# Optimization experiments

Hardware: AMD Instinct MI355X
Metric: run time of the kernel (lower is better)

Reference implementation:

```python
import jax, jax.numpy as jnp
import numpy as np

D_EMBEDDING = 512
DIMENSION = 64
B, N = 8, 2048


def setup_inputs() -> dict:
    key = jax.random.key(0)
    k1, k2, k3, k4, k5, k6 = jax.random.split(key, 6)
    bound = 1.0 / np.sqrt(D_EMBEDDING)  # nn.Linear default init
    return {
        "key_input": jax.random.normal(k1, (B, N, D_EMBEDDING), jnp.float32),
        "query_input": jax.random.normal(k2, (B, N, D_EMBEDDING), jnp.float32),
        "value_input": jax.random.normal(k3, (B, N, D_EMBEDDING), jnp.float32),
        "padding_mask": jnp.zeros((B, 1, N), dtype=bool),
        "masked_attention": 1,
        "W_key": jax.random.uniform(k4, (D_EMBEDDING, DIMENSION), jnp.float32, -bound, bound),
        "W_query": jax.random.uniform(k5, (D_EMBEDDING, DIMENSION), jnp.float32, -bound, bound),
        "W_value": jax.random.uniform(k6, (D_EMBEDDING, DIMENSION), jnp.float32, -bound, bound),
    }


def reference(key_input, query_input, value_input, padding_mask, masked_attention,
              W_key, W_query, W_value):
    # NOTE: faithful to the original torch code, which uses self.key for
    # Q, K AND V (W_query / W_value are unused by forward) and scales by
    # sqrt(D_i) where D_i is the INPUT embedding dim (512), not the head dim.
    B_, N_, D_i = value_input.shape
    K = key_input @ W_key      # [B, N, d]
    Q = query_input @ W_key    # [B, N, d]
    V = value_input @ W_key    # [B, N, d]

    scores = jnp.einsum("bqd,bkd->bqk", Q, K) / jnp.sqrt(jnp.float32(D_i))
    neg_inf = jnp.float32(-jnp.inf)
    scores = jnp.where(padding_mask, neg_inf, scores)
    if masked_attention:
        causal = jnp.tril(jnp.ones((N_, N_), dtype=bool))  # [N, N]
        scores = jnp.where(causal, scores, neg_inf)
    probs = jax.nn.softmax(scores, axis=-1)
    return jnp.einsum("bqk,bkd->bqd", probs, V)
```

## Files before the change

### kernel.cpp

```cpp
#include <hip/hip_runtime.h>
#include <hip/hip_bf16.h>
#include <math.h>

#define D_EMB 512
#define HD 64
#define BB 8
#define NN 2048
#define MROWS (BB*NN)

typedef short short8  __attribute__((ext_vector_type(8)));
typedef short short4v __attribute__((ext_vector_type(4)));
typedef float f32x4   __attribute__((ext_vector_type(4)));

#define QSCALE 0.063758708f

__device__ __forceinline__ short f2bf(float x){
    unsigned u = __float_as_uint(x);
    unsigned r = (u + 0x7fffu + ((u >> 16) & 1u)) >> 16;
    return (short)r;
}
__device__ __forceinline__ float bf2f(short b){
    return __uint_as_float(((unsigned)(unsigned short)b) << 16);
}
__device__ __forceinline__ unsigned pkbf(float a, float b){
    __hip_bfloat162 h = __float22bfloat162_rn(make_float2(a, b));
    unsigned u; __builtin_memcpy(&u, &h, 4); return u;
}
__device__ __forceinline__ void gl16(const short* g, short* l){
    __builtin_amdgcn_global_load_lds(
        (const __attribute__((address_space(1))) unsigned*)g,
        (__attribute__((address_space(3))) unsigned*)l, 16, 0, 0);
}

__global__ __launch_bounds__(256)
void wt_kernel(const float* __restrict__ W, short* __restrict__ Wtf){
    for (int idx = blockIdx.x * 256 + threadIdx.x; idx < D_EMB*HD; idx += 64*256){
        int k = idx >> 6, n = idx & 63;
        int off = (((k >> 5)*4 + (n >> 4))*64 + ((k >> 3) & 3)*16 + (n & 15))*8 + (k & 7);
        Wtf[off] = f2bf(W[idx]);
    }
}

__global__ __launch_bounds__(256, 2)
void proj_kernel(const float* __restrict__ Xq, const float* __restrict__ Xk,
                 const float* __restrict__ Xv, const short* __restrict__ Wtf,
                 short* __restrict__ Qb, short* __restrict__ Kb,
                 short* __restrict__ Vt)
{
    __shared__ short sW[D_EMB*HD];
    const int tid = threadIdx.x;
    const int lane = tid & 63;
    const int lc = lane & 15, quad = lane >> 4;
    const int wid = blockIdx.x * 4 + (tid >> 6);
    const int m0 = wid * 16;
    const int tensor = m0 >> 14;
    const int rloc = m0 & (MROWS - 1);
    const float* X = (tensor == 0) ? Xq : (tensor == 1 ? Xk : Xv);
    const float* xbase = X + (size_t)(rloc + lc)*D_EMB + quad*8;

    float4 xa[4][2];
#pragma unroll
    for (int p = 0; p < 4; ++p){
        xa[p][0] = *(const float4*)(xbase + p*32);
        xa[p][1] = *(const float4*)(xbase + p*32 + 4);
    }

#pragma unroll
    for (int pass = 0; pass < 16; ++pass)
        gl16(Wtf + pass*2048 + tid*8, sW + pass*2048 + tid*8);

    f32x4 acc[4];
#pragma unroll
    for (int t = 0; t < 4; ++t)
#pragma unroll
        for (int r = 0; r < 4; ++r) acc[t][r] = 0.f;

    __syncthreads();

#pragma unroll
    for (int c16 = 0; c16 < 16; ++c16){
        float4 f0 = xa[c16 & 3][0], f1 = xa[c16 & 3][1];
        if (c16 < 12){
            xa[c16 & 3][0] = *(const float4*)(xbase + (c16+4)*32);
            xa[c16 & 3][1] = *(const float4*)(xbase + (c16+4)*32 + 4);
        }
        union { short8 s8; unsigned u[4]; } a;
        a.u[0] = pkbf(f0.x, f0.y); a.u[1] = pkbf(f0.z, f0.w);
        a.u[2] = pkbf(f1.x, f1.y); a.u[3] = pkbf(f1.z, f1.w);
#pragma unroll
        for (int t = 0; t < 4; ++t){
            short8 bf = *(const short8*)&sW[((c16*4 + t)*64 + lane)*8];
            acc[t] = __builtin_amdgcn_mfma_f32_16x16x32_bf16(a.s8, bf, acc[t], 0,0,0);
        }
    }

    if (tensor == 0){
#pragma unroll
        for (int t = 0; t < 4; ++t)
#pragma unroll
            for (int r = 0; r < 4; ++r)
                Qb[(size_t)(rloc + quad*4 + r)*HD + t*16 + lc] = f2bf(acc[t][r] * QSCALE);
    } else if (tensor == 1){
#pragma unroll
        for (int t = 0; t < 4; ++t)
#pragma unroll
            for (int r = 0; r < 4; ++r){
                const int R = rloc + quad*4 + r;
                const int nin = R & 63;
                const int off = ((R >> 6) << 12) + nin*64
                              + ((((t << 1) | (lc >> 3)) ^ (nin & 7)) << 3) + (lc & 7);
                Kb[off] = f2bf(acc[t][r]);
            }
    } else {
#pragma unroll
        for (int t = 0; t < 4; ++t)
#pragma unroll
            for (int r = 0; r < 4; ++r){
                const int R = rloc + quad*4 + r;
                const int nin = R & 63;
                const int d = t*16 + lc;
                const int off = ((R >> 6) << 12) + d*64
                              + (((nin >> 3) ^ (lc & 7)) << 3) + (nin & 7);
                Vt[off] = f2bf(acc[t][r]);
            }
    }
}

template<int SH>
__global__ __launch_bounds__(256)
void attn_part(const short* __restrict__ Qb, const short* __restrict__ Kb,
               const short* __restrict__ Vt, const unsigned char* __restrict__ pad,
               const int* __restrict__ mflag, float* __restrict__ out,
               float* __restrict__ Lp, short* __restrict__ Op)
{
    constexpr int M   = 1 << SH;
    constexpr int NG  = 32 / M;
    constexpr int UPB = M * NG * (NG + 1) / 2;
    constexpr int PPB = UPB - M;

    __shared__ short sK[2][4096];
    __shared__ short sV[2][4096];
    __shared__ short sP[4][16][80];

    const int tid = threadIdx.x, lane = tid & 63, lc = lane & 15, quad = lane >> 4, w = tid >> 6;
    const int unit = blockIdx.x;
    const int b = unit / UPB;
    const int rem = unit - b * UPB;
    int a = 0;
    while (rem >= (M * (a + 1) * (a + 2)) / 2) ++a;
    const int u = rem - M * a * (a + 1) / 2;
    const int C = a + 1;
    const int r = u / C, c = u - r * C;
    const int j = a * M + r;
    const int q0 = j * 64;

    const bool causal = (mflag[0] != 0);
    const int T = causal ? (j + 1) : 32;
    const int qq = (T + C - 1) / C;
    const int t0 = c * qq;
    const int t1 = min(t0 + qq, T);
    const int tb = b * 32;
    const unsigned char* padb = pad + (size_t)b * NN;

    const short* qrow = Qb + ((size_t)b * NN + q0 + w*16 + lc) * HD;
    const short8 qf0 = *(const short8*)(qrow + quad * 8);
    const short8 qf1 = *(const short8*)(qrow + 32 + quad * 8);

    f32x4 o[4];
#pragma unroll
    for (int t = 0; t < 4; ++t)
#pragma unroll
        for (int rr = 0; rr < 4; ++rr) o[t][rr] = 0.f;
    float lacc = 0.f;

    {
        const short* gk = Kb + ((size_t)(tb + t0) << 12) + w*1024 + lane*8;
        const short* gv = Vt + ((size_t)(tb + t0) << 12) + w*1024 + lane*8;
        short* lk = &sK[0][w*1024 + lane*8];
        short* lv = &sV[0][w*1024 + lane*8];
        gl16(gk, lk); gl16(gk + 512, lk + 512);
        gl16(gv, lv); gl16(gv + 512, lv + 512);
    }

    int buf = 0;
    const int sw = lc & 7;
    for (int kt = t0; kt < t1; ++kt, buf ^= 1){
        __syncthreads();
        if (kt + 1 < t1){
            const short* gk = Kb + ((size_t)(tb + kt + 1) << 12) + w*1024 + lane*8;
            const short* gv = Vt + ((size_t)(tb + kt + 1) << 12) + w*1024 + lane*8;
            short* lk = &sK[buf ^ 1][w*1024 + lane*8];
            short* lv = &sV[buf ^ 1][w*1024 + lane*8];
            gl16(gk, lk); gl16(gk + 512, lk + 512);
            gl16(gv, lv); gl16(gv + 512, lv + 512);
        }
        const int k0 = kt * 64;
        short8 kf0[4], kf1[4], vf0[4], vf1[4];
#pragma unroll
        for (int t = 0; t < 4; ++t){
            const int row = (t*16 + lc) * 64;
            kf0[t] = *(const short8*)&sK[buf][row + ((quad ^ sw) << 3)];
            kf1[t] = *(const short8*)&sK[buf][row + (((quad + 4) ^ sw) << 3)];
            vf0[t] = *(const short8*)&sV[buf][row + ((quad ^ sw) << 3)];
            vf1[t] = *(const short8*)&sV[buf][row + (((quad + 4) ^ sw) << 3)];
        }
        f32x4 st[4];
#pragma unroll
        for (int t = 0; t < 4; ++t){
#pragma unroll
            for (int rr = 0; rr < 4; ++rr) st[t][rr] = 0.f;
            st[t] = __builtin_amdgcn_mfma_f32_16x16x32_bf16(kf0[t], qf0, st[t], 0,0,0);
            st[t] = __builtin_amdgcn_mfma_f32_16x16x32_bf16(kf1[t], qf1, st[t], 0,0,0);
        }
        const bool dg = causal && (kt == j);
        const int thr = q0 + w*16 + lc - k0;
#pragma unroll
        for (int t = 0; t < 4; ++t){
            uchar4 pb = *(const uchar4*)(padb + k0 + t*16 + quad*4);
            float e[4];
#pragma unroll
            for (int rr = 0; rr < 4; ++rr){
                float v = st[t][rr];
                const unsigned char pr = (rr==0)?pb.x:(rr==1)?pb.y:(rr==2)?pb.z:pb.w;
                const int nloc = t*16 + quad*4 + rr;
                if (pr || (dg && nloc > thr)) v = -INFINITY;
                e[rr] = exp2f(v);
                lacc += e[rr];
            }
            union { short4v s4; unsigned uu[2]; } pk;
            pk.uu[0] = pkbf(e[0], e[1]);
            pk.uu[1] = pkbf(e[2], e[3]);
            *(short4v*)&sP[w][lc][t*16 + quad*4] = pk.s4;
        }
        const short8 pf0 = *(const short8*)&sP[w][lc][quad*8];
        const short8 pf1 = *(const short8*)&sP[w][lc][32 + quad*8];
#pragma unroll
        for (int t = 0; t < 4; ++t){
            o[t] = __builtin_amdgcn_mfma_f32_16x16x32_bf16(pf0, vf0[t], o[t], 0,0,0);
            o[t] = __builtin_amdgcn_mfma_f32_16x16x32_bf16(pf1, vf1[t], o[t], 0,0,0);
        }
    }

    lacc += __shfl_xor(lacc, 16);
    lacc += __shfl_xor(lacc, 32);

    if (C == 1){
        float linv[4];
#pragma unroll
        for (int rr = 0; rr < 4; ++rr) linv[rr] = 1.f / __shfl(lacc, quad*4 + rr);
#pragma unroll
        for (int rr = 0; rr < 4; ++rr){
            float* orow = out + ((size_t)b*NN + q0 + w*16 + quad*4 + rr)*HD;
#pragma unroll
            for (int t = 0; t < 4; ++t) orow[t*16 + lc] = o[t][rr] * linv[rr];
        }
    } else {
        const int pu = b*PPB + (M*a*(a+1)/2 - M) + r*C + c;
        short* op = Op + (size_t)pu * 4096;
#pragma unroll
        for (int t = 0; t < 4; ++t)
#pragma unroll
            for (int rr = 0; rr < 4; ++rr)
                op[(w*16 + quad*4 + rr)*64 + t*16 + lc] = f2bf(o[t][rr]);
        if (lane < 16) Lp[pu*64 + w*16 + lane] = lacc;
    }
}

template<int SH>
__global__ __launch_bounds__(256)
void attn_combine(const float* __restrict__ Lp, const short* __restrict__ Op,
                  float* __restrict__ out)
{
    constexpr int M    = 1 << SH;
    constexpr int UPB  = M * (32/M) * (32/M + 1) / 2;
    constexpr int PPB  = UPB - M;
    constexpr int NSTR = 32 - M;
    const int tid = threadIdx.x, lane = tid & 63;
    const int unit = blockIdx.x;
    const int per_b = NSTR * 16;
    const int b = unit / per_b;
    const int rem = unit - b * per_b;
    const int j = M + (rem >> 4);
    const int row = (rem & 15) * 4 + (tid >> 6);
    const int a = j >> SH;
    const int C = a + 1;
    const int r = j - a * M;
    const int pu0 = b*PPB + (M*a*(a+1)/2 - M) + r*C;

    float l = 0.f, acc = 0.f;
    for (int cc = 0; cc < C; ++cc){
        l   += Lp[(pu0 + cc)*64 + row];
        acc += bf2f(Op[(size_t)(pu0 + cc)*4096 + row*64 + lane]);
    }
    out[((size_t)b*NN + j*64 + row)*HD + lane] = acc / l;
}

extern "C" void kernel_launch(void* const* d_in, const int* in_sizes, int n_in,
                              void* d_out, int out_size, void* d_ws, size_t ws_size,
                              hipStream_t stream) {
    const float* key_in   = (const float*)d_in[0];
    const float* query_in = (const float*)d_in[1];
    const float* value_in = (const float*)d_in[2];
    const unsigned char* pad = (const unsigned char*)d_in[3];
    const int* mflag      = (const int*)d_in[4];
    const float* Wk       = (const float*)d_in[5];

    short* Qb = (short*)d_ws;
    short* Kb = Qb + (size_t)MROWS*HD;
    short* Vt = Kb + (size_t)MROWS*HD;
    short* Wtf = Vt + (size_t)MROWS*HD;
    float* Lp = (float*)(Wtf + D_EMB*HD);

    wt_kernel<<<64, 256, 0, stream>>>(Wk, Wtf);
    proj_kernel<<<768, 256, 0, stream>>>(query_in, key_in, value_in, Wtf, Qb, Kb, Vt);

    if (ws_size >= (size_t)15818752){
        short* Op = (short*)(Lp + 1120*64);
        attn_part<2><<<1152, 256, 0, stream>>>(Qb, Kb, Vt, pad, mflag, (float*)d_out, Lp, Op);
        attn_combine<2><<<BB*28*16, 256, 0, stream>>>(Lp, Op, (float*)d_out);
    } else {
        short* Op = (short*)(Lp + 576*64);
        attn_part<3><<<640, 256, 0, stream>>>(Qb, Kb, Vt, pad, mflag, (float*)d_out, Lp, Op);
        attn_combine<3><<<BB*24*16, 256, 0, stream>>>(Lp, Op, (float*)d_out);
    }
}
```

Before: 171.9 us.

## Restructure projection: weights in registers, double-buffered X tiles via async LDS loads

The projection kernel no longer stages the whole 64 KB bf16 weight matrix in LDS per block. Each wave now keeps its 16-column slice of W in registers. Each block streams six 16-row X tiles through a double-buffered, XOR-swizzled fp32 LDS buffer filled with global_load_lds, so the next tile loads while the current one runs MFMA. This removes the redundant per-block weight copy and overlaps input loads with compute. In exchange it uses more registers, and each wave now does only one 16x16 output tile per group.

```diff
diff --git a/kernel.cpp b/kernel.cpp
--- a/kernel.cpp
+++ b/kernel.cpp
@@ -26,7 +26,7 @@
     __hip_bfloat162 h = __float22bfloat162_rn(make_float2(a, b));
     unsigned u; __builtin_memcpy(&u, &h, 4); return u;
 }
-__device__ __forceinline__ void gl16(const short* g, short* l){
+__device__ __forceinline__ void gl16(const void* g, void* l){
     __builtin_amdgcn_global_load_lds(
         (const __attribute__((address_space(1))) unsigned*)g,
         (__attribute__((address_space(3))) unsigned*)l, 16, 0, 0);
@@ -47,82 +47,97 @@
                  short* __restrict__ Qb, short* __restrict__ Kb,
                  short* __restrict__ Vt)
 {
-    __shared__ short sW[D_EMB*HD];
+    __shared__ float sX[2][16][512];
     const int tid = threadIdx.x;
     const int lane = tid & 63;
     const int lc = lane & 15, quad = lane >> 4;
-    const int wid = blockIdx.x * 4 + (tid >> 6);
-    const int m0 = wid * 16;
-    const int tensor = m0 >> 14;
-    const int rloc = m0 & (MROWS - 1);
-    const float* X = (tensor == 0) ? Xq : (tensor == 1 ? Xk : Xv);
-    const float* xbase = X + (size_t)(rloc + lc)*D_EMB + quad*8;
-
-    float4 xa[4][2];
-#pragma unroll
-    for (int p = 0; p < 4; ++p){
-        xa[p][0] = *(const float4*)(xbase + p*32);
-        xa[p][1] = *(const float4*)(xbase + p*32 + 4);
-    }
-
-#pragma unroll
-    for (int pass = 0; pass < 16; ++pass)
-        gl16(Wtf + pass*2048 + tid*8, sW + pass*2048 + tid*8);
-
-    f32x4 acc[4];
-#pragma unroll
-    for (int t = 0; t < 4; ++t)
-#pragma unroll
-        for (int r = 0; r < 4; ++r) acc[t][r] = 0.f;
-
-    __syncthreads();
-
-#pragma unroll
-    for (int c16 = 0; c16 < 16; ++c16){
-        float4 f0 = xa[c16 & 3][0], f1 = xa[c16 & 3][1];
-        if (c16 < 12){
-            xa[c16 & 3][0] = *(const float4*)(xbase + (c16+4)*32);
-            xa[c16 & 3][1] = *(const float4*)(xbase + (c16+4)*32 + 4);
-        }
-        union { short8 s8; unsigned u[4]; } a;
-        a.u[0] = pkbf(f0.x, f0.y); a.u[1] = pkbf(f0.z, f0.w);
-        a.u[2] = pkbf(f1.x, f1.y); a.u[3] = pkbf(f1.z, f1.w);
-#pragma unroll
-        for (int t = 0; t < 4; ++t){
-            short8 bf = *(const short8*)&sW[((c16*4 + t)*64 + lane)*8];
-            acc[t] = __builtin_amdgcn_mfma_f32_16x16x32_bf16(a.s8, bf, acc[t], 0,0,0);
-        }
-    }
-
-    if (tensor == 0){
-#pragma unroll
-        for (int t = 0; t < 4; ++t)
+    const int w = tid >> 6;
+
+    short8 bfW[16];
+#pragma unroll
+    for (int c = 0; c < 16; ++c)
+        bfW[c] = *(const short8*)(Wtf + (size_t)(((c*4 + w)*64 + lane)*8));
+
+    const int s_pj   = (tid & 127) >> 1;
+    const int s_half = tid & 1;
+
+    const int g0 = blockIdx.x * 6;
+
+    {
+        const int grp = g0;
+        const int tensor = grp >> 10;
+        const int rloc = (grp << 4) & (MROWS - 1);
+        const float* X = (tensor == 0) ? Xq : (tensor == 1 ? Xk : Xv);
+#pragma unroll
+        for (int pass = 0; pass < 8; ++pass){
+            const int row = pass*2 + (tid >> 7);
+            const int j = (s_pj & ~7) | ((s_pj ^ row) & 7);
+            gl16(X + (size_t)(rloc + row)*D_EMB + j*8 + s_half*4,
+                 &sX[0][0][0] + pass*1024 + tid*4);
+        }
+    }
+
+    for (int g = 0; g < 6; ++g){
+        const int grp = g0 + g;
+        const int cur = g & 1;
+        __syncthreads();
+        if (g + 1 < 6){
+            const int ng = grp + 1;
+            const int tensor = ng >> 10;
+            const int rloc = (ng << 4) & (MROWS - 1);
+            const float* X = (tensor == 0) ? Xq : (tensor == 1 ? Xk : Xv);
+#pragma unroll
+            for (int pass = 0; pass < 8; ++pass){
+                const int row = pass*2 + (tid >> 7);
+                const int j = (s_pj & ~7) | ((s_pj ^ row) & 7);
+                gl16(X + (size_t)(rloc + row)*D_EMB + j*8 + s_half*4,
+                     &sX[cur ^ 1][0][0] + pass*1024 + tid*4);
+            }
+        }
+
+        f32x4 acc;
+#pragma unroll
+        for (int r = 0; r < 4; ++r) acc[r] = 0.f;
+
+#pragma unroll
+        for (int c16 = 0; c16 < 16; ++c16){
+            const int j = c16*4 + quad;
+            const int pj = (j & ~7) | ((j ^ lc) & 7);
+            const float* p = &sX[cur][lc][0] + pj*8;
+            float4 f0 = *(const float4*)p;
+            float4 f1 = *(const float4*)(p + 4);
+            union { short8 s8; unsigned u[4]; } a;
+            a.u[0] = pkbf(f0.x, f0.y); a.u[1] = pkbf(f0.z, f0.w);
+            a.u[2] = pkbf(f1.x, f1.y); a.u[3] = pkbf(f1.z, f1.w);
+            acc = __builtin_amdgcn_mfma_f32_16x16x32_bf16(a.s8, bfW[c16], acc, 0,0,0);
+        }
+
+        const int tensor = grp >> 10;
+        const int rloc = (grp << 4) & (MROWS - 1);
+        if (tensor == 0){
 #pragma unroll
             for (int r = 0; r < 4; ++r)
-                Qb[(size_t)(rloc + quad*4 + r)*HD + t*16 + lc] = f2bf(acc[t][r] * QSCALE);
-    } else if (tensor == 1){
-#pragma unroll
-        for (int t = 0; t < 4; ++t)
+                Qb[(size_t)(rloc + quad*4 + r)*HD + w*16 + lc] = f2bf(acc[r] * QSCALE);
+        } else if (tensor == 1){
 #pragma unroll
             for (int r = 0; r < 4; ++r){
                 const int R = rloc + quad*4 + r;
                 const int nin = R & 63;
                 const int off = ((R >> 6) << 12) + nin*64
-                              + ((((t << 1) | (lc >> 3)) ^ (nin & 7)) << 3) + (lc & 7);
-                Kb[off] = f2bf(acc[t][r]);
+                              + ((((w << 1) | (lc >> 3)) ^ (nin & 7)) << 3) + (lc & 7);
+                Kb[off] = f2bf(acc[r]);
             }
-    } else {
-#pragma unroll
-        for (int t = 0; t < 4; ++t)
+        } else {
 #pragma unroll
             for (int r = 0; r < 4; ++r){
                 const int R = rloc + quad*4 + r;
                 const int nin = R & 63;
-                const int d = t*16 + lc;
+                const int d = w*16 + lc;
                 const int off = ((R >> 6) << 12) + d*64
                               + (((nin >> 3) ^ (lc & 7)) << 3) + (nin & 7);
-                Vt[off] = f2bf(acc[t][r]);
+                Vt[off] = f2bf(acc[r]);
             }
+        }
     }
 }
 
@@ -312,7 +327,7 @@
     float* Lp = (float*)(Wtf + D_EMB*HD);
 
     wt_kernel<<<64, 256, 0, stream>>>(Wk, Wtf);
-    proj_kernel<<<768, 256, 0, stream>>>(query_in, key_in, value_in, Wtf, Qb, Kb, Vt);
+    proj_kernel<<<512, 256, 0, stream>>>(query_in, key_in, value_in, Wtf, Qb, Kb, Vt);
 
     if (ws_size >= (size_t)15818752){
         short* Op = (short*)(Lp + 1120*64);
```

Result: faster. 163.6 us (-4.8%).
